# Optimization experiments

Hardware: AMD Instinct MI355X
Metric: run time of the kernel (lower is better)

Reference implementation:

```python
import jax, jax.numpy as jnp
import numpy as np

H = 16        # query heads
HK = 8        # kv heads
D = 128       # head dim
HID = 2048    # hidden size
FF = 6144     # mlp intermediate
THETA = 1e6   # rope base (qwen3)
EPS = 1e-6
T = 2048      # total tokens


def rmsnorm(x, w):
    return x * jax.lax.rsqrt(jnp.mean(x * x, axis=-1, keepdims=True) + EPS) * w


def rope(pos, x):
    # x: [T, h, D], rotate-half RoPE
    half = D // 2
    inv = 1.0 / (THETA ** (jnp.arange(half, dtype=jnp.float32) / half))
    freqs = pos.astype(jnp.float32)[:, None] * inv          # [T, half]
    cos = jnp.cos(freqs)[:, None, :]
    sin = jnp.sin(freqs)[:, None, :]
    x1, x2 = x[..., :half], x[..., half:]
    return jnp.concatenate([x1 * cos - x2 * sin, x2 * cos + x1 * sin], axis=-1)


def setup_inputs() -> dict:
    key = jax.random.key(0)
    ks = jax.random.split(key, 12)
    s = 0.02
    return {
        "positions": jnp.arange(T, dtype=jnp.int32),
        "hidden_states": jax.random.normal(ks[0], (T, HID), dtype=jnp.float32),
        "wq": jax.random.normal(ks[1], (H * D, HID), dtype=jnp.float32) * s,
        "wk": jax.random.normal(ks[2], (HK * D, HID), dtype=jnp.float32) * s,
        "wv": jax.random.normal(ks[3], (HK * D, HID), dtype=jnp.float32) * s,
        "wo": jax.random.normal(ks[4], (HID, H * D), dtype=jnp.float32) * s,
        "q_norm_w": jnp.ones((D,), dtype=jnp.float32),
        "k_norm_w": jnp.ones((D,), dtype=jnp.float32),
        "ln1_w": jnp.ones((HID,), dtype=jnp.float32),
        "ln2_w": jnp.ones((HID,), dtype=jnp.float32),
        "w_gate": jax.random.normal(ks[5], (FF, HID), dtype=jnp.float32) * s,
        "w_up": jax.random.normal(ks[6], (FF, HID), dtype=jnp.float32) * s,
        "w_down": jax.random.normal(ks[7], (HID, FF), dtype=jnp.float32) * s,
    }


def reference(positions, hidden_states, wq, wk, wv, wo, q_norm_w, k_norm_w,
              ln1_w, ln2_w, w_gate, w_up, w_down):
    t = hidden_states.shape[0]
    residual = hidden_states
    h = rmsnorm(hidden_states, ln1_w)
    q = (h @ wq.T).reshape(t, H, D)
    k = (h @ wk.T).reshape(t, HK, D)
    v = (h @ wv.T).reshape(t, HK, D)
    q = rmsnorm(q, q_norm_w)
    k = rmsnorm(k, k_norm_w)
    q = rope(positions, q)
    k = rope(positions, k)
    # GQA: expand kv heads to query heads
    g = H // HK
    kr = jnp.repeat(k, g, axis=1)  # [t, H, D]
    vr = jnp.repeat(v, g, axis=1)
    scores = jnp.einsum('thd,shd->hts', q, kr) * (D ** -0.5)
    causal = positions[:, None] >= positions[None, :]
    scores = jnp.where(causal[None], scores, jnp.finfo(scores.dtype).min)
    p = jax.nn.softmax(scores, axis=-1)
    o = jnp.einsum('hts,shd->thd', p, vr).reshape(t, H * D)
    h = residual + o @ wo.T
    residual = h
    h = rmsnorm(h, ln2_w)
    h = (jax.nn.silu(h @ w_gate.T) * (h @ w_up.T)) @ w_down.T
    return residual + h
```

## Files before the change

### kernel.cpp

```cpp
#include <hip/hip_runtime.h>
#include <hip/hip_bf16.h>
#include <stdint.h>

namespace {

constexpr int kT   = 2048;
constexpr int kHid = 2048;
constexpr int kH   = 16;
constexpr int kHK  = 8;
constexpr int kD   = 128;
constexpr int kFF  = 6144;

using bf16x8 = __attribute__((ext_vector_type(8))) short;
using f32x4  = __attribute__((ext_vector_type(4))) float;

__device__ __forceinline__ float bf2f(unsigned short u) {
    return __uint_as_float(((unsigned)u) << 16);
}
__device__ __forceinline__ unsigned short f2bf(float f) {
    unsigned u = __float_as_uint(f);
    return (unsigned short)((u + 0x7fffu + ((u >> 16) & 1u)) >> 16);
}
__device__ __forceinline__ void gload_lds16(const void* g, void* l) {
    __builtin_amdgcn_global_load_lds(
        (__attribute__((address_space(1))) void*)g,
        (__attribute__((address_space(3))) void*)l, 16, 0, 0);
}
__device__ __forceinline__ f32x4 mf(bf16x8 a, bf16x8 b, f32x4 c) {
    return __builtin_amdgcn_mfma_f32_16x16x32_bf16(a, b, c, 0, 0, 0);
}

__global__ __launch_bounds__(256)
void cvt_f32_bf16(const float* __restrict__ src, unsigned short* __restrict__ dst, int n4) {
    int i = blockIdx.x * 256 + threadIdx.x;
    if (i < n4) {
        float4 v = ((const float4*)src)[i];
        ushort4 o;
        o.x = f2bf(v.x); o.y = f2bf(v.y); o.z = f2bf(v.z); o.w = f2bf(v.w);
        ((ushort4*)dst)[i] = o;
    }
}

__global__ __launch_bounds__(256)
void reduce4(const float* __restrict__ p0, const float* __restrict__ p1,
             const float* __restrict__ p2, const float* __restrict__ p3,
             const float* __restrict__ res, float* __restrict__ out, int n4) {
    int i = blockIdx.x * 256 + threadIdx.x;
    if (i < n4) {
        float4 a = ((const float4*)p0)[i];
        float4 b = ((const float4*)p1)[i];
        float4 c = ((const float4*)p2)[i];
        float4 d = ((const float4*)p3)[i];
        float4 r = ((const float4*)res)[i];
        float4 o;
        o.x = a.x + b.x + c.x + d.x + r.x;
        o.y = a.y + b.y + c.y + d.y + r.y;
        o.z = a.z + b.z + c.z + d.z + r.z;
        o.w = a.w + b.w + c.w + d.w + r.w;
        ((float4*)out)[i] = o;
    }
}

__global__ __launch_bounds__(256)
void rmsnorm_k(const float* __restrict__ x, const float* __restrict__ w,
               unsigned short* __restrict__ out) {
    const int row = blockIdx.x;
    const int tid = threadIdx.x;
    const float4* xr = (const float4*)(x + (size_t)row * kHid);
    float4 v0 = xr[tid];
    float4 v1 = xr[tid + 256];
    float ss = v0.x*v0.x + v0.y*v0.y + v0.z*v0.z + v0.w*v0.w
             + v1.x*v1.x + v1.y*v1.y + v1.z*v1.z + v1.w*v1.w;
#pragma unroll
    for (int m = 1; m < 64; m <<= 1) ss += __shfl_xor(ss, m);
    __shared__ float red[4];
    if ((tid & 63) == 0) red[tid >> 6] = ss;
    __syncthreads();
    float tot = red[0] + red[1] + red[2] + red[3];
    float rs = rsqrtf(tot * (1.0f / kHid) + 1e-6f);
    const float4* wv = (const float4*)w;
    float4 w0 = wv[tid], w1 = wv[tid + 256];
    ushort4 o0, o1;
    o0.x = f2bf(v0.x * rs * w0.x); o0.y = f2bf(v0.y * rs * w0.y);
    o0.z = f2bf(v0.z * rs * w0.z); o0.w = f2bf(v0.w * rs * w0.w);
    o1.x = f2bf(v1.x * rs * w1.x); o1.y = f2bf(v1.y * rs * w1.y);
    o1.z = f2bf(v1.z * rs * w1.z); o1.w = f2bf(v1.w * rs * w1.w);
    ushort4* orow = (ushort4*)(out + (size_t)row * kHid);
    orow[tid] = o0;
    orow[tid + 256] = o1;
}

template <int EPI>
__global__ __launch_bounds__(512, 2)
void gemm256(const unsigned short* __restrict__ A,
             const unsigned short* __restrict__ B,
             void* __restrict__ C,
             const float* __restrict__ Res,
             const unsigned short* __restrict__ G,
             int M, int N, int K, int KS,
             float* __restrict__ p0, float* __restrict__ p1,
             float* __restrict__ p2, float* __restrict__ p3) {
    __shared__ unsigned short smem[2][4][128 * 64];

    const int tid  = threadIdx.x;
    const int lane = tid & 63;
    const int l15  = lane & 15;
    const int g4   = lane >> 4;
    const int wid  = tid >> 6;
    const int wr   = wid >> 2;
    const int wc   = wid & 3;
    const int bm   = blockIdx.y * 256;
    const int bn   = blockIdx.x * 256;
    const int kb   = (EPI == 4) ? blockIdx.z * KS : 0;
    const int NT   = ((EPI == 4) ? KS : K) >> 6;
    const int NI   = NT >> 1;

    f32x4 acc[8][4] = {};

    auto stage = [&](int b, int reg, int t) {
        const unsigned short* Base = (reg < 2) ? A : B;
        const int br = ((reg < 2) ? bm : bn) + (reg & 1) * 128;
#pragma unroll
        for (int i = 0; i < 2; ++i) {
            int ch   = tid + i * 512;
            int row  = ch >> 3;
            int slot = (ch & 7) ^ (row & 7);
            gload_lds16(Base + (size_t)(br + row) * K + kb + t * 64 + slot * 8,
                        (char*)&smem[b][reg][0] + ch * 16);
        }
    };
    auto rdA = [&](int b, int m, int ks) {
        int row = m * 16 + l15;
        return *(const bf16x8*)((const char*)&smem[b][wr][0]
               + row * 128 + (((ks * 4 + g4) ^ (row & 7)) * 16));
    };
    auto rdB = [&](int b, int n, int ks) {
        int row = wc * 64 + n * 16 + l15;
        return *(const bf16x8*)((const char*)&smem[b][2 + (row >> 7)][0]
               + (row & 127) * 128 + (((ks * 4 + g4) ^ (row & 7)) * 16));
    };

    stage(0, 2, 0); stage(0, 3, 0); stage(0, 0, 0); stage(0, 1, 0);
    stage(1, 2, 1); stage(1, 3, 1); stage(1, 0, 1);
    asm volatile("s_waitcnt vmcnt(6)" ::: "memory");
    __builtin_amdgcn_s_barrier();

    for (int i = 0; i < NI; ++i) {
        const int e  = 2 * i;
        const int o  = e + 1;
        const bool pf = (e + 2 < NT);
        bf16x8 af[4][2], bfr[4][2];

#pragma unroll
        for (int m = 0; m < 4; ++m) { af[m][0] = rdA(0, m, 0); af[m][1] = rdA(0, m, 1); }
#pragma unroll
        for (int n = 0; n < 4; ++n) { bfr[n][0] = rdB(0, n, 0); bfr[n][1] = rdB(0, n, 1); }
        stage(1, 1, o);
        __builtin_amdgcn_s_barrier();
        asm volatile("s_waitcnt lgkmcnt(0)" ::: "memory");
        __builtin_amdgcn_sched_barrier(0);
        __builtin_amdgcn_s_setprio(1);
#pragma unroll
        for (int m = 0; m < 4; ++m)
#pragma unroll
            for (int n = 0; n < 2; ++n) {
                acc[m][n] = mf(af[m][0], bfr[n][0], acc[m][n]);
                acc[m][n] = mf(af[m][1], bfr[n][1], acc[m][n]);
            }
        __builtin_amdgcn_s_setprio(0);
        __builtin_amdgcn_s_barrier();

        if (pf) stage(0, 2, e + 2);
        __builtin_amdgcn_s_barrier();
        __builtin_amdgcn_s_setprio(1);
#pragma unroll
        for (int m = 0; m < 4; ++m)
#pragma unroll
            for (int n = 2; n < 4; ++n) {
                acc[m][n] = mf(af[m][0], bfr[n][0], acc[m][n]);
                acc[m][n] = mf(af[m][1], bfr[n][1], acc[m][n]);
            }
        __builtin_amdgcn_s_setprio(0);
        __builtin_amdgcn_s_barrier();

#pragma unroll
        for (int m = 0; m < 4; ++m) { af[m][0] = rdA(0, 4 + m, 0); af[m][1] = rdA(0, 4 + m, 1); }
        if (pf) stage(0, 3, e + 2);
        __builtin_amdgcn_s_barrier();
        asm volatile("s_waitcnt lgkmcnt(0)" ::: "memory");
        __builtin_amdgcn_sched_barrier(0);
        __builtin_amdgcn_s_setprio(1);
#pragma unroll
        for (int m = 0; m < 4; ++m)
#pragma unroll
            for (int n = 0; n < 2; ++n) {
                acc[4 + m][n] = mf(af[m][0], bfr[n][0], acc[4 + m][n]);
                acc[4 + m][n] = mf(af[m][1], bfr[n][1], acc[4 + m][n]);
            }
        __builtin_amdgcn_s_setprio(0);
        __builtin_amdgcn_s_barrier();

        if (pf) stage(0, 0, e + 2);
        __builtin_amdgcn_s_barrier();
        __builtin_amdgcn_s_setprio(1);
#pragma unroll
        for (int m = 0; m < 4; ++m)
#pragma unroll
            for (int n = 2; n < 4; ++n) {
                acc[4 + m][n] = mf(af[m][0], bfr[n][0], acc[4 + m][n]);
                acc[4 + m][n] = mf(af[m][1], bfr[n][1], acc[4 + m][n]);
            }
        __builtin_amdgcn_s_setprio(0);
        if (pf) asm volatile("s_waitcnt vmcnt(6)" ::: "memory");
        else    asm volatile("s_waitcnt vmcnt(0)" ::: "memory");
        __builtin_amdgcn_s_barrier();

#pragma unroll
        for (int m = 0; m < 4; ++m) { af[m][0] = rdA(1, m, 0); af[m][1] = rdA(1, m, 1); }
#pragma unroll
        for (int n = 0; n < 4; ++n) { bfr[n][0] = rdB(1, n, 0); bfr[n][1] = rdB(1, n, 1); }
        if (pf) stage(0, 1, e + 2);
        __builtin_amdgcn_s_barrier();
        asm volatile("s_waitcnt lgkmcnt(0)" ::: "memory");
        __builtin_amdgcn_sched_barrier(0);
        __builtin_amdgcn_s_setprio(1);
#pragma unroll
        for (int m = 0; m < 4; ++m)
#pragma unroll
            for (int n = 0; n < 2; ++n) {
                acc[m][n] = mf(af[m][0], bfr[n][0], acc[m][n]);
                acc[m][n] = mf(af[m][1], bfr[n][1], acc[m][n]);
            }
        __builtin_amdgcn_s_setprio(0);
        __builtin_amdgcn_s_barrier();

        if (pf) stage(1, 2, o + 2);
        __builtin_amdgcn_s_barrier();
        __builtin_amdgcn_s_setprio(1);
#pragma unroll
        for (int m = 0; m < 4; ++m)
#pragma unroll
            for (int n = 2; n < 4; ++n) {
                acc[m][n] = mf(af[m][0], bfr[n][0], acc[m][n]);
                acc[m][n] = mf(af[m][1], bfr[n][1], acc[m][n]);
            }
        __builtin_amdgcn_s_setprio(0);
        __builtin_amdgcn_s_barrier();

#pragma unroll
        for (int m = 0; m < 4; ++m) { af[m][0] = rdA(1, 4 + m, 0); af[m][1] = rdA(1, 4 + m, 1); }
        if (pf) stage(1, 3, o + 2);
        __builtin_amdgcn_s_barrier();
        asm volatile("s_waitcnt lgkmcnt(0)" ::: "memory");
        __builtin_amdgcn_sched_barrier(0);
        __builtin_amdgcn_s_setprio(1);
#pragma unroll
        for (int m = 0; m < 4; ++m)
#pragma unroll
            for (int n = 0; n < 2; ++n) {
                acc[4 + m][n] = mf(af[m][0], bfr[n][0], acc[4 + m][n]);
                acc[4 + m][n] = mf(af[m][1], bfr[n][1], acc[4 + m][n]);
            }
        __builtin_amdgcn_s_setprio(0);
        __builtin_amdgcn_s_barrier();

        if (pf) stage(1, 0, o + 2);
        __builtin_amdgcn_s_barrier();
        __builtin_amdgcn_s_setprio(1);
#pragma unroll
        for (int m = 0; m < 4; ++m)
#pragma unroll
            for (int n = 2; n < 4; ++n) {
                acc[4 + m][n] = mf(af[m][0], bfr[n][0], acc[4 + m][n]);
                acc[4 + m][n] = mf(af[m][1], bfr[n][1], acc[4 + m][n]);
            }
        __builtin_amdgcn_s_setprio(0);
        if (pf) asm volatile("s_waitcnt vmcnt(6)" ::: "memory");
        __builtin_amdgcn_s_barrier();
    }

    float* P = nullptr;
    if (EPI == 4) {
        const int z = blockIdx.z;
        P = (z == 0) ? p0 : (z == 1) ? p1 : (z == 2) ? p2 : p3;
    }
#pragma unroll
    for (int m = 0; m < 8; ++m) {
#pragma unroll
        for (int n = 0; n < 4; ++n) {
            int row = bm + wr * 128 + m * 16 + g4 * 4;
            int col = bn + wc * 64 + n * 16 + l15;
#pragma unroll
            for (int r = 0; r < 4; ++r) {
                size_t idx = (size_t)(row + r) * N + col;
                float v = acc[m][n][r];
                if (EPI == 0) {
                    ((float*)C)[idx] = v;
                } else if (EPI == 1) {
                    ((unsigned short*)C)[idx] = f2bf(v);
                } else if (EPI == 2) {
                    ((float*)C)[idx] = v + Res[idx];
                } else if (EPI == 3) {
                    float g = bf2f(G[idx]);
                    ((unsigned short*)C)[idx] = f2bf(g / (1.0f + __expf(-g)) * v);
                } else {
                    P[idx] = v;
                }
            }
        }
    }
}

__global__ __launch_bounds__(512, 2)
void gemm_gu(const unsigned short* __restrict__ A,
             const unsigned short* __restrict__ WGp,
             const unsigned short* __restrict__ WUp,
             unsigned short* __restrict__ OUT) {
    __shared__ unsigned short smem[2][4][128 * 64];

    const int tid  = threadIdx.x;
    const int lane = tid & 63;
    const int l15  = lane & 15;
    const int g4   = lane >> 4;
    const int wid  = tid >> 6;
    const int wr   = wid >> 1;
    const int wc   = wid & 1;
    const int bm   = blockIdx.y * 256;
    const int bn2  = blockIdx.x * 128;
    const int K    = kHid;
    const int NT   = K >> 6;
    const int NI   = NT >> 1;

    f32x4 accg[4][4] = {};
    f32x4 accu[4][4] = {};

    auto stage = [&](int b, int reg, int t) {
        const unsigned short* Base = (reg == 2) ? WGp : (reg == 3) ? WUp : A;
        const int br = (reg < 2) ? (bm + reg * 128) : bn2;
#pragma unroll
        for (int i = 0; i < 2; ++i) {
            int ch   = tid + i * 512;
            int row  = ch >> 3;
            int slot = (ch & 7) ^ (row & 7);
            gload_lds16(Base + (size_t)(br + row) * K + t * 64 + slot * 8,
                        (char*)&smem[b][reg][0] + ch * 16);
        }
    };
    auto rdA = [&](int b, int m, int ks) {
        int rt  = wr * 64 + m * 16 + l15;
        int row = rt & 127;
        return *(const bf16x8*)((const char*)&smem[b][rt >> 7][0]
               + row * 128 + (((ks * 4 + g4) ^ (row & 7)) * 16));
    };
    auto rdB = [&](int b, int reg, int n, int ks) {
        int row = wc * 64 + n * 16 + l15;
        return *(const bf16x8*)((const char*)&smem[b][reg][0]
               + row * 128 + (((ks * 4 + g4) ^ (row & 7)) * 16));
    };

    stage(0, 2, 0); stage(0, 3, 0); stage(0, 0, 0); stage(0, 1, 0);
    stage(1, 2, 1); stage(1, 0, 1); stage(1, 1, 1);
    asm volatile("s_waitcnt vmcnt(6)" ::: "memory");
    __builtin_amdgcn_s_barrier();

    for (int i = 0; i < NI; ++i) {
        const int e  = 2 * i;
        const int o  = e + 1;
        const bool pf = (e + 2 < NT);
        bf16x8 af[4][2], bg[4][2], bu[4][2];

#pragma unroll
        for (int m = 0; m < 4; ++m) { af[m][0] = rdA(0, m, 0); af[m][1] = rdA(0, m, 1); }
#pragma unroll
        for (int n = 0; n < 4; ++n) { bg[n][0] = rdB(0, 2, n, 0); bg[n][1] = rdB(0, 2, n, 1); }
        stage(1, 3, o);
        __builtin_amdgcn_s_barrier();
        asm volatile("s_waitcnt lgkmcnt(0)" ::: "memory");
        __builtin_amdgcn_sched_barrier(0);
        __builtin_amdgcn_s_setprio(1);
#pragma unroll
        for (int m = 0; m < 4; ++m)
#pragma unroll
            for (int n = 0; n < 2; ++n) {
                accg[m][n] = mf(af[m][0], bg[n][0], accg[m][n]);
                accg[m][n] = mf(af[m][1], bg[n][1], accg[m][n]);
            }
        __builtin_amdgcn_s_setprio(0);
        __builtin_amdgcn_s_barrier();

        if (pf) stage(0, 2, e + 2);
        __builtin_amdgcn_s_barrier();
        __builtin_amdgcn_s_setprio(1);
#pragma unroll
        for (int m = 0; m < 4; ++m)
#pragma unroll
            for (int n = 2; n < 4; ++n) {
                accg[m][n] = mf(af[m][0], bg[n][0], accg[m][n]);
                accg[m][n] = mf(af[m][1], bg[n][1], accg[m][n]);
            }
        __builtin_amdgcn_s_setprio(0);
        __builtin_amdgcn_s_barrier();

#pragma unroll
        for (int n = 0; n < 4; ++n) { bu[n][0] = rdB(0, 3, n, 0); bu[n][1] = rdB(0, 3, n, 1); }
        if (pf) stage(0, 0, e + 2);
        __builtin_amdgcn_s_barrier();
        asm volatile("s_waitcnt lgkmcnt(0)" ::: "memory");
        __builtin_amdgcn_sched_barrier(0);
        __builtin_amdgcn_s_setprio(1);
#pragma unroll
        for (int m = 0; m < 4; ++m)
#pragma unroll
            for (int n = 0; n < 2; ++n) {
                accu[m][n] = mf(af[m][0], bu[n][0], accu[m][n]);
                accu[m][n] = mf(af[m][1], bu[n][1], accu[m][n]);
            }
        __builtin_amdgcn_s_setprio(0);
        __builtin_amdgcn_s_barrier();

        if (pf) stage(0, 1, e + 2);
        __builtin_amdgcn_s_barrier();
        __builtin_amdgcn_s_setprio(1);
#pragma unroll
        for (int m = 0; m < 4; ++m)
#pragma unroll
            for (int n = 2; n < 4; ++n) {
                accu[m][n] = mf(af[m][0], bu[n][0], accu[m][n]);
                accu[m][n] = mf(af[m][1], bu[n][1], accu[m][n]);
            }
        __builtin_amdgcn_s_setprio(0);
        if (pf) asm volatile("s_waitcnt vmcnt(6)" ::: "memory");
        else    asm volatile("s_waitcnt vmcnt(0)" ::: "memory");
        __builtin_amdgcn_s_barrier();

#pragma unroll
        for (int m = 0; m < 4; ++m) { af[m][0] = rdA(1, m, 0); af[m][1] = rdA(1, m, 1); }
#pragma unroll
        for (int n = 0; n < 4; ++n) { bg[n][0] = rdB(1, 2, n, 0); bg[n][1] = rdB(1, 2, n, 1); }
        if (pf) stage(0, 3, e + 2);
        __builtin_amdgcn_s_barrier();
        asm volatile("s_waitcnt lgkmcnt(0)" ::: "memory");
        __builtin_amdgcn_sched_barrier(0);
        __builtin_amdgcn_s_setprio(1);
#pragma unroll
        for (int m = 0; m < 4; ++m)
#pragma unroll
            for (int n = 0; n < 2; ++n) {
                accg[m][n] = mf(af[m][0], bg[n][0], accg[m][n]);
                accg[m][n] = mf(af[m][1], bg[n][1], accg[m][n]);
            }
        __builtin_amdgcn_s_setprio(0);
        __builtin_amdgcn_s_barrier();

        if (pf) stage(1, 2, o + 2);
        __builtin_amdgcn_s_barrier();
        __builtin_amdgcn_s_setprio(1);
#pragma unroll
        for (int m = 0; m < 4; ++m)
#pragma unroll
            for (int n = 2; n < 4; ++n) {
                accg[m][n] = mf(af[m][0], bg[n][0], accg[m][n]);
                accg[m][n] = mf(af[m][1], bg[n][1], accg[m][n]);
            }
        __builtin_amdgcn_s_setprio(0);
        __builtin_amdgcn_s_barrier();

#pragma unroll
        for (int n = 0; n < 4; ++n) { bu[n][0] = rdB(1, 3, n, 0); bu[n][1] = rdB(1, 3, n, 1); }
        if (pf) stage(1, 0, o + 2);
        __builtin_amdgcn_s_barrier();
        asm volatile("s_waitcnt lgkmcnt(0)" ::: "memory");
        __builtin_amdgcn_sched_barrier(0);
        __builtin_amdgcn_s_setprio(1);
#pragma unroll
        for (int m = 0; m < 4; ++m)
#pragma unroll
            for (int n = 0; n < 2; ++n) {
                accu[m][n] = mf(af[m][0], bu[n][0], accu[m][n]);
                accu[m][n] = mf(af[m][1], bu[n][1], accu[m][n]);
            }
        __builtin_amdgcn_s_setprio(0);
        __builtin_amdgcn_s_barrier();

        if (pf) stage(1, 1, o + 2);
        __builtin_amdgcn_s_barrier();
        __builtin_amdgcn_s_setprio(1);
#pragma unroll
        for (int m = 0; m < 4; ++m)
#pragma unroll
            for (int n = 2; n < 4; ++n) {
                accu[m][n] = mf(af[m][0], bu[n][0], accu[m][n]);
                accu[m][n] = mf(af[m][1], bu[n][1], accu[m][n]);
            }
        __builtin_amdgcn_s_setprio(0);
        if (pf) asm volatile("s_waitcnt vmcnt(6)" ::: "memory");
        __builtin_amdgcn_s_barrier();
    }

#pragma unroll
    for (int m = 0; m < 4; ++m) {
#pragma unroll
        for (int n = 0; n < 4; ++n) {
            int row = bm + wr * 64 + m * 16 + g4 * 4;
            int col = bn2 + wc * 64 + n * 16 + l15;
#pragma unroll
            for (int r = 0; r < 4; ++r) {
                float g = accg[m][n][r];
                float u = accu[m][n][r];
                OUT[(size_t)(row + r) * kFF + col] = f2bf(g / (1.0f + __expf(-g)) * u);
            }
        }
    }
}

__global__ __launch_bounds__(256)
void qknorm_rope(const float* __restrict__ qp0, const float* __restrict__ qp1,
                 const int* __restrict__ positions,
                 const float* __restrict__ qnw, const float* __restrict__ knw,
                 unsigned short* __restrict__ Qo, unsigned short* __restrict__ Ko) {
    const int t    = blockIdx.x;
    const int j    = blockIdx.y * 4 + (threadIdx.x >> 6);
    const int lane = threadIdx.x & 63;
    const size_t base = (size_t)t * 4096 + j * 128;
    float x1 = qp0[base + lane] + qp1[base + lane];
    float x2 = qp0[base + lane + 64] + qp1[base + lane + 64];
    float ss = x1 * x1 + x2 * x2;
#pragma unroll
    for (int m = 1; m < 64; m <<= 1) ss += __shfl_xor(ss, m);
    float rs = rsqrtf(ss * (1.0f / 128.0f) + 1e-6f);
    const float* w = (j < 16) ? qnw : knw;
    float n1 = x1 * rs * w[lane];
    float n2 = x2 * rs * w[lane + 64];
    float inv = powf(1.0e6f, -(float)lane * (1.0f / 64.0f));
    float fr = (float)positions[t] * inv;
    float sn, cs;
    sincosf(fr, &sn, &cs);
    float o1 = n1 * cs - n2 * sn;
    float o2 = n2 * cs + n1 * sn;
    if (j < 16) {
        unsigned short* d = Qo + (size_t)t * (kH * kD) + j * kD;
        d[lane] = f2bf(o1);
        d[lane + 64] = f2bf(o2);
    } else {
        unsigned short* d = Ko + (size_t)t * (kHK * kD) + (j - 16) * kD;
        d[lane] = f2bf(o1);
        d[lane + 64] = f2bf(o2);
    }
}

__global__ __launch_bounds__(256)
void vtrans(const float* __restrict__ qp0, const float* __restrict__ qp1,
            unsigned short* __restrict__ Vt) {
    __shared__ float tile[32][33];
    const int t0 = blockIdx.x * 32;
    const int d0 = blockIdx.y * 32;
    const int tc = threadIdx.x & 31;
    const int tr = threadIdx.x >> 5;
#pragma unroll
    for (int i = 0; i < 4; ++i) {
        int trow = tr + i * 8;
        size_t idx = (size_t)(t0 + trow) * 4096 + 3072 + d0 + tc;
        tile[trow][tc] = qp0[idx] + qp1[idx];
    }
    __syncthreads();
#pragma unroll
    for (int i = 0; i < 4; ++i) {
        int drow = tr + i * 8;
        Vt[(size_t)(d0 + drow) * kT + t0 + tc] = f2bf(tile[tc][drow]);
    }
}

__global__ __launch_bounds__(512, 4)
void attn_fwd5(const unsigned short* __restrict__ Q,
               const unsigned short* __restrict__ Kc,
               const unsigned short* __restrict__ Vt,
               unsigned short* __restrict__ O) {
    __shared__ unsigned short Kb[2][64 * 128];
    __shared__ unsigned short Vb[2][128 * 64];
    __shared__ float MergeML[4][2][64];

    const int tid  = threadIdx.x;
    const int lane = tid & 63;
    const int l15  = lane & 15;
    const int g4   = lane >> 4;
    const int wid  = tid >> 6;
    const int s    = wid & 1;
    const int grp  = wid >> 1;
    const int hs   = grp >> 1;
    const int qsub = grp & 1;
    const int hkk  = blockIdx.x;
    const int h    = hkk * 2 + hs;
    const int nby  = gridDim.y;
    const int by   = blockIdx.y;
    const int byl  = (by & 1) ? (nby - 1 - (by >> 1)) : (by >> 1);
    const int q0   = byl * 32 + qsub * 16;
    const int nch  = byl / 2 + 1;
    const int c0   = (nch + 1) >> 1;
    const int myn  = s ? (nch - c0) : c0;
    const int qi   = q0 + l15;
    const int vt   = grp * 64 + lane;

    const int addrA = ((g4 & 1) * 32 + l15) * 4;
    const int addrB = addrA + 64;
    const int addrQ = g4 * 80;
    const bool hb   = (g4 >> 1) != 0;

    bf16x8 qf[4];
#pragma unroll
    for (int ks = 0; ks < 4; ++ks)
        qf[ks] = *(const bf16x8*)(Q + (size_t)(q0 + l15) * (kH * kD) + h * kD + ks * 32 + g4 * 8);

    f32x4 oacc[8] = {};
    float mrun = -3e38f, lrun = 0.f;
    const float scale = 0.08838834764831845f;

    auto stage = [&](int kv0) {
#pragma unroll
        for (int i = 0; i < 4; ++i) {
            int ch  = vt + i * 256;
            int row = ch >> 4;
            int c16 = ch & 15;
            gload_lds16(Kc + (size_t)(kv0 + row) * (kHK * kD) + hkk * kD
                            + ((c16 ^ (row & 7)) * 8),
                        (char*)Kb[s] + ch * 16);
        }
#pragma unroll
        for (int i = 0; i < 4; ++i) {
            int ch  = vt + i * 256;
            int row = ch >> 3;
            int c8  = ch & 7;
            gload_lds16(Vt + (size_t)(hkk * kD + row) * kT + kv0
                            + ((c8 ^ (row & 7)) * 8),
                        (char*)Vb[s] + ch * 16);
        }
    };

    for (int c = 0; c < c0; ++c) {
        const bool act = c < myn;
        const int kv0 = (s ? (c0 + c) : c) * 64;
        if (act) stage(kv0);
        asm volatile("s_waitcnt vmcnt(0)" ::: "memory");
        __builtin_amdgcn_s_barrier();
        __builtin_amdgcn_sched_barrier(0);

        if (act) {
            f32x4 sa[4] = {};
            __builtin_amdgcn_s_setprio(1);
#pragma unroll
            for (int hh = 0; hh < 4; ++hh) {
                const int row = hh * 16 + l15;
#pragma unroll
                for (int ks = 0; ks < 4; ++ks) {
                    bf16x8 kf = *(const bf16x8*)((const char*)Kb[s]
                                  + row * 256 + (((ks * 4 + g4) ^ (row & 7)) * 16));
                    sa[hh] = mf(kf, qf[ks], sa[hh]);
                }
            }
            __builtin_amdgcn_s_setprio(0);

            float sv[4][4];
#pragma unroll
            for (int hh = 0; hh < 4; ++hh)
#pragma unroll
                for (int r = 0; r < 4; ++r)
                    sv[hh][r] = sa[hh][r] * scale;
            if (kv0 + 63 > q0) {
#pragma unroll
                for (int hh = 0; hh < 4; ++hh)
#pragma unroll
                    for (int r = 0; r < 4; ++r) {
                        int ki = kv0 + hh * 16 + g4 * 4 + r;
                        if (ki > qi) sv[hh][r] = -3e38f;
                    }
            }

            float m16;
            {
                float a = fmaxf(fmaxf(sv[0][0], sv[0][1]), fmaxf(sv[0][2], sv[0][3]));
                float b2 = fmaxf(fmaxf(sv[1][0], sv[1][1]), fmaxf(sv[1][2], sv[1][3]));
                float c2 = fmaxf(fmaxf(sv[2][0], sv[2][1]), fmaxf(sv[2][2], sv[2][3]));
                float d2 = fmaxf(fmaxf(sv[3][0], sv[3][1]), fmaxf(sv[3][2], sv[3][3]));
                m16 = fmaxf(fmaxf(a, b2), fmaxf(c2, d2));
            }
            m16 = fmaxf(m16, __shfl_xor(m16, 16));
            m16 = fmaxf(m16, __shfl_xor(m16, 32));

            if (__any(m16 > mrun)) {
                float mnew = fmaxf(mrun, m16);
                float corr = __expf(mrun - mnew);
                mrun = mnew;
                lrun *= corr;
                float cr[4];
#pragma unroll
                for (int r = 0; r < 4; ++r)
                    cr[r] = __int_as_float(__builtin_amdgcn_ds_bpermute(
                                addrQ + 4 * r, __float_as_int(corr)));
#pragma unroll
                for (int c2 = 0; c2 < 8; ++c2)
#pragma unroll
                    for (int r = 0; r < 4; ++r)
                        oacc[c2][r] *= cr[r];
            }

            float p[4][4];
            float ps = 0.f;
#pragma unroll
            for (int hh = 0; hh < 4; ++hh)
#pragma unroll
                for (int r = 0; r < 4; ++r) {
                    float pe = __expf(sv[hh][r] - mrun);
                    p[hh][r] = pe;
                    ps += pe;
                }
            ps += __shfl_xor(ps, 16);
            ps += __shfl_xor(ps, 32);
            lrun += ps;

            unsigned pk[4][2];
#pragma unroll
            for (int hh = 0; hh < 4; ++hh) {
                asm("v_cvt_pk_bf16_f32 %0, %1, %2"
                    : "=v"(pk[hh][0]) : "v"(p[hh][0]), "v"(p[hh][1]));
                asm("v_cvt_pk_bf16_f32 %0, %1, %2"
                    : "=v"(pk[hh][1]) : "v"(p[hh][2]), "v"(p[hh][3]));
            }
            int ex[4][2][2];
#pragma unroll
            for (int hh = 0; hh < 4; ++hh)
#pragma unroll
                for (int ii = 0; ii < 2; ++ii) {
                    ex[hh][ii][0] = __builtin_amdgcn_ds_bpermute(addrA, (int)pk[hh][ii]);
                    ex[hh][ii][1] = __builtin_amdgcn_ds_bpermute(addrB, (int)pk[hh][ii]);
                }
            union { int w[4]; bf16x8 v; } pu0, pu1;
#pragma unroll
            for (int jw = 0; jw < 4; ++jw) {
                pu0.w[jw] = hb ? ex[1][jw & 1][jw >> 1] : ex[0][jw & 1][jw >> 1];
                pu1.w[jw] = hb ? ex[3][jw & 1][jw >> 1] : ex[2][jw & 1][jw >> 1];
            }
            bf16x8 pa0 = pu0.v;
            bf16x8 pa1 = pu1.v;

            __builtin_amdgcn_s_setprio(1);
#pragma unroll
            for (int c2 = 0; c2 < 8; ++c2) {
                const int d = c2 * 16 + l15;
                bf16x8 vf0 = *(const bf16x8*)((const char*)Vb[s]
                              + d * 128 + ((g4 ^ (d & 7)) * 16));
                oacc[c2] = mf(pa0, vf0, oacc[c2]);
                bf16x8 vf1 = *(const bf16x8*)((const char*)Vb[s]
                              + d * 128 + ((((4 + g4) ^ (d & 7))) * 16));
                oacc[c2] = mf(pa1, vf1, oacc[c2]);
            }
            __builtin_amdgcn_s_setprio(0);
        }
        __builtin_amdgcn_s_barrier();
    }

    float* KbF = (float*)&Kb[0][0];
    if (s == 1) {
        MergeML[grp][0][lane] = mrun;
        MergeML[grp][1][lane] = lrun;
#pragma unroll
        for (int c2 = 0; c2 < 8; ++c2)
#pragma unroll
            for (int r = 0; r < 4; ++r)
                KbF[grp * 2048 + (c2 * 4 + r) * 64 + lane] = oacc[c2][r];
    }
    asm volatile("s_waitcnt lgkmcnt(0)" ::: "memory");
    __builtin_amdgcn_s_barrier();

    if (s == 0) {
        float m1 = MergeML[grp][0][lane];
        float l1 = MergeML[grp][1][lane];
        float mg = fmaxf(mrun, m1);
        float a0 = __expf(mrun - mg);
        float a1 = __expf(m1 - mg);
        float L  = lrun * a0 + l1 * a1;
        float ar0[4], ar1[4], Lr[4];
#pragma unroll
        for (int r = 0; r < 4; ++r) {
            ar0[r] = __int_as_float(__builtin_amdgcn_ds_bpermute(
                         addrQ + 4 * r, __float_as_int(a0)));
            ar1[r] = __int_as_float(__builtin_amdgcn_ds_bpermute(
                         addrQ + 4 * r, __float_as_int(a1)));
            Lr[r]  = __int_as_float(__builtin_amdgcn_ds_bpermute(
                         addrQ + 4 * r, __float_as_int(L)));
        }
#pragma unroll
        for (int c2 = 0; c2 < 8; ++c2)
#pragma unroll
            for (int r = 0; r < 4; ++r) {
                float oex = KbF[grp * 2048 + (c2 * 4 + r) * 64 + lane];
                float v = (oacc[c2][r] * ar0[r] + oex * ar1[r]) / Lr[r];
                O[(size_t)(q0 + g4 * 4 + r) * (kH * kD) + h * kD + c2 * 16 + l15] = f2bf(v);
            }
    }
}

}

extern "C" void kernel_launch(void* const* d_in, const int* in_sizes, int n_in,
                              void* d_out, int out_size, void* d_ws, size_t ws_size,
                              hipStream_t stream) {
    (void)in_sizes; (void)n_in; (void)out_size; (void)ws_size;

    const int*   positions = (const int*)  d_in[0];
    const float* hidden    = (const float*)d_in[1];
    const float* wq  = (const float*)d_in[2];
    const float* wk  = (const float*)d_in[3];
    const float* wv  = (const float*)d_in[4];
    const float* wo  = (const float*)d_in[5];
    const float* qnw = (const float*)d_in[6];
    const float* knw = (const float*)d_in[7];
    const float* ln1 = (const float*)d_in[8];
    const float* ln2 = (const float*)d_in[9];
    const float* wg  = (const float*)d_in[10];
    const float* wu  = (const float*)d_in[11];
    const float* wd  = (const float*)d_in[12];

    char* ws = (char*)d_ws;
    unsigned short* WQKV = (unsigned short*)(ws + 0);
    unsigned short* WO   = (unsigned short*)(ws + 16777216);
    unsigned short* WG   = (unsigned short*)(ws + 25165824);
    unsigned short* WU   = (unsigned short*)(ws + 50331648);
    unsigned short* WD   = (unsigned short*)(ws + 75497472);
    unsigned short* XN1  = (unsigned short*)(ws + 100663296);
    unsigned short* OATT = (unsigned short*)(ws + 109051904);
    float*          H1   = (float*)(ws + 117440512);
    unsigned short* XN2  = (unsigned short*)(ws + 134217728);
    unsigned short* QB   = (unsigned short*)(ws + 176160768);
    unsigned short* KB   = (unsigned short*)(ws + 184549376);
    unsigned short* VT   = (unsigned short*)(ws + 188743680);
    unsigned short* ACT  = (unsigned short*)(ws + 167772160);

    float* QP0 = (float*)(ws + 142606336);
    float* QP1 = (float*)(ws + 109051904);
    float* OP0 = (float*)(ws + 142606336);
    float* OP1 = (float*)(ws + 159383552);
    float* OP2 = (float*)(ws + 176160768);
    float* OP3 = (float*)(ws + 0);
    float* DP0 = (float*)(ws + 0);
    float* DP1 = (float*)(ws + 16777216);
    float* DP2 = (float*)(ws + 33554432);
    float* DP3 = (float*)(ws + 142606336);

    auto cvt = [&](const float* s, unsigned short* dst, size_t n) {
        int n4 = (int)(n / 4);
        cvt_f32_bf16<<<dim3((n4 + 255) / 256), dim3(256), 0, stream>>>(s, dst, n4);
    };

    cvt(wq, WQKV,                 (size_t)kH  * kD * kHid);
    cvt(wk, WQKV + 2048 * kHid,   (size_t)kHK * kD * kHid);
    cvt(wv, WQKV + 3072 * kHid,   (size_t)kHK * kD * kHid);
    cvt(wo, WO,                   (size_t)kHid * kH * kD);
    cvt(wg, WG,                   (size_t)kFF * kHid);
    cvt(wu, WU,                   (size_t)kFF * kHid);
    cvt(wd, WD,                   (size_t)kHid * kFF);

    rmsnorm_k<<<dim3(kT), dim3(256), 0, stream>>>(hidden, ln1, XN1);

    gemm256<4><<<dim3(4096 / 256, kT / 256, 2), dim3(512), 0, stream>>>(
        XN1, WQKV, nullptr, nullptr, nullptr, kT, 4096, kHid, 1024,
        QP0, QP1, QP0, QP0);

    qknorm_rope<<<dim3(kT, 6), dim3(256), 0, stream>>>(
        QP0, QP1, positions, qnw, knw, QB, KB);
    vtrans<<<dim3(kT / 32, 1024 / 32), dim3(256), 0, stream>>>(QP0, QP1, VT);

    attn_fwd5<<<dim3(kHK, kT / 32), dim3(512), 0, stream>>>(QB, KB, VT, OATT);

    gemm256<4><<<dim3(kHid / 256, kT / 256, 4), dim3(512), 0, stream>>>(
        OATT, WO, nullptr, nullptr, nullptr, kT, kHid, kHid, 512,
        OP0, OP1, OP2, OP3);
    reduce4<<<dim3(kT * kHid / 4 / 256), dim3(256), 0, stream>>>(
        OP0, OP1, OP2, OP3, hidden, H1, kT * kHid / 4);

    rmsnorm_k<<<dim3(kT), dim3(256), 0, stream>>>(H1, ln2, XN2);

    gemm_gu<<<dim3(kFF / 128, kT / 256), dim3(512), 0, stream>>>(XN2, WG, WU, ACT);

    gemm256<4><<<dim3(kHid / 256, kT / 256, 4), dim3(512), 0, stream>>>(
        ACT, WD, nullptr, nullptr, nullptr, kT, kHid, kFF, 1536,
        DP0, DP1, DP2, DP3);
    reduce4<<<dim3(kT * kHid / 4 / 256), dim3(256), 0, stream>>>(
        DP0, DP1, DP2, DP3, H1, (float*)d_out, kT * kHid / 4);
}
```

Baseline: 413.2 us.

## Shrink GEMM M-tile to 128 and cut split-K partials

Replaces the 256x256 split-K GEMM with a 128x256 tile variant. The QKV projection now runs without split-K and writes a single fp32 buffer directly. The O-projection and down-projection drop from four K-splits to two, so a reduce2 kernel replaces reduce4. Halving the M tile doubles the block count, which keeps parallelism while cutting partial-sum traffic and reduction work. The cost is lower data reuse per block, since each B tile is loaded for only 128 rows, and more LDS traffic relative to MFMA work.

```diff
diff --git a/kernel.cpp b/kernel.cpp
--- a/kernel.cpp
+++ b/kernel.cpp
@@ -42,21 +42,18 @@
 }
 
 __global__ __launch_bounds__(256)
-void reduce4(const float* __restrict__ p0, const float* __restrict__ p1,
-             const float* __restrict__ p2, const float* __restrict__ p3,
+void reduce2(const float* __restrict__ p0, const float* __restrict__ p1,
              const float* __restrict__ res, float* __restrict__ out, int n4) {
     int i = blockIdx.x * 256 + threadIdx.x;
     if (i < n4) {
         float4 a = ((const float4*)p0)[i];
         float4 b = ((const float4*)p1)[i];
-        float4 c = ((const float4*)p2)[i];
-        float4 d = ((const float4*)p3)[i];
         float4 r = ((const float4*)res)[i];
         float4 o;
-        o.x = a.x + b.x + c.x + d.x + r.x;
-        o.y = a.y + b.y + c.y + d.y + r.y;
-        o.z = a.z + b.z + c.z + d.z + r.z;
-        o.w = a.w + b.w + c.w + d.w + r.w;
+        o.x = a.x + b.x + r.x;
+        o.y = a.y + b.y + r.y;
+        o.z = a.z + b.z + r.z;
+        o.w = a.w + b.w + r.w;
         ((float4*)out)[i] = o;
     }
 }
@@ -92,15 +89,12 @@
 
 template <int EPI>
 __global__ __launch_bounds__(512, 2)
-void gemm256(const unsigned short* __restrict__ A,
+void gemm128(const unsigned short* __restrict__ A,
              const unsigned short* __restrict__ B,
              void* __restrict__ C,
-             const float* __restrict__ Res,
-             const unsigned short* __restrict__ G,
              int M, int N, int K, int KS,
-             float* __restrict__ p0, float* __restrict__ p1,
-             float* __restrict__ p2, float* __restrict__ p3) {
-    __shared__ unsigned short smem[2][4][128 * 64];
+             float* __restrict__ p0, float* __restrict__ p1) {
+    __shared__ unsigned short smem[2][3][128 * 64];
 
     const int tid  = threadIdx.x;
     const int lane = tid & 63;
@@ -109,17 +103,17 @@
     const int wid  = tid >> 6;
     const int wr   = wid >> 2;
     const int wc   = wid & 3;
-    const int bm   = blockIdx.y * 256;
+    const int bm   = blockIdx.y * 128;
     const int bn   = blockIdx.x * 256;
     const int kb   = (EPI == 4) ? blockIdx.z * KS : 0;
     const int NT   = ((EPI == 4) ? KS : K) >> 6;
     const int NI   = NT >> 1;
 
-    f32x4 acc[8][4] = {};
+    f32x4 acc[4][4] = {};
 
     auto stage = [&](int b, int reg, int t) {
-        const unsigned short* Base = (reg < 2) ? A : B;
-        const int br = ((reg < 2) ? bm : bn) + (reg & 1) * 128;
+        const unsigned short* Base = (reg == 0) ? A : B;
+        const int br = (reg == 0) ? bm : bn + (reg - 1) * 128;
 #pragma unroll
         for (int i = 0; i < 2; ++i) {
             int ch   = tid + i * 512;
@@ -130,19 +124,19 @@
         }
     };
     auto rdA = [&](int b, int m, int ks) {
-        int row = m * 16 + l15;
-        return *(const bf16x8*)((const char*)&smem[b][wr][0]
+        int row = wr * 64 + m * 16 + l15;
+        return *(const bf16x8*)((const char*)&smem[b][0][0]
                + row * 128 + (((ks * 4 + g4) ^ (row & 7)) * 16));
     };
     auto rdB = [&](int b, int n, int ks) {
         int row = wc * 64 + n * 16 + l15;
-        return *(const bf16x8*)((const char*)&smem[b][2 + (row >> 7)][0]
+        return *(const bf16x8*)((const char*)&smem[b][1 + (row >> 7)][0]
                + (row & 127) * 128 + (((ks * 4 + g4) ^ (row & 7)) * 16));
     };
 
-    stage(0, 2, 0); stage(0, 3, 0); stage(0, 0, 0); stage(0, 1, 0);
-    stage(1, 2, 1); stage(1, 3, 1); stage(1, 0, 1);
-    asm volatile("s_waitcnt vmcnt(6)" ::: "memory");
+    stage(0, 1, 0); stage(0, 2, 0); stage(0, 0, 0);
+    stage(1, 1, 1); stage(1, 2, 1);
+    asm volatile("s_waitcnt vmcnt(4)" ::: "memory");
     __builtin_amdgcn_s_barrier();
 
     for (int i = 0; i < NI; ++i) {
@@ -155,18 +149,27 @@
         for (int m = 0; m < 4; ++m) { af[m][0] = rdA(0, m, 0); af[m][1] = rdA(0, m, 1); }
 #pragma unroll
         for (int n = 0; n < 4; ++n) { bfr[n][0] = rdB(0, n, 0); bfr[n][1] = rdB(0, n, 1); }
-        stage(1, 1, o);
+        stage(1, 0, o);
         __builtin_amdgcn_s_barrier();
         asm volatile("s_waitcnt lgkmcnt(0)" ::: "memory");
         __builtin_amdgcn_sched_barrier(0);
         __builtin_amdgcn_s_setprio(1);
 #pragma unroll
-        for (int m = 0; m < 4; ++m)
-#pragma unroll
-            for (int n = 0; n < 2; ++n) {
-                acc[m][n] = mf(af[m][0], bfr[n][0], acc[m][n]);
-                acc[m][n] = mf(af[m][1], bfr[n][1], acc[m][n]);
-            }
+        for (int m = 0; m < 4; ++m) {
+            acc[m][0] = mf(af[m][0], bfr[0][0], acc[m][0]);
+            acc[m][0] = mf(af[m][1], bfr[0][1], acc[m][0]);
+        }
+        __builtin_amdgcn_s_setprio(0);
+        __builtin_amdgcn_s_barrier();
+
+        if (pf) stage(0, 1, e + 2);
+        __builtin_amdgcn_s_barrier();
+        __builtin_amdgcn_s_setprio(1);
+#pragma unroll
+        for (int m = 0; m < 4; ++m) {
+            acc[m][1] = mf(af[m][0], bfr[1][0], acc[m][1]);
+            acc[m][1] = mf(af[m][1], bfr[1][1], acc[m][1]);
+        }
         __builtin_amdgcn_s_setprio(0);
         __builtin_amdgcn_s_barrier();
 
@@ -174,63 +177,49 @@
         __builtin_amdgcn_s_barrier();
         __builtin_amdgcn_s_setprio(1);
 #pragma unroll
-        for (int m = 0; m < 4; ++m)
-#pragma unroll
-            for (int n = 2; n < 4; ++n) {
-                acc[m][n] = mf(af[m][0], bfr[n][0], acc[m][n]);
-                acc[m][n] = mf(af[m][1], bfr[n][1], acc[m][n]);
-            }
-        __builtin_amdgcn_s_setprio(0);
-        __builtin_amdgcn_s_barrier();
-
-#pragma unroll
-        for (int m = 0; m < 4; ++m) { af[m][0] = rdA(0, 4 + m, 0); af[m][1] = rdA(0, 4 + m, 1); }
-        if (pf) stage(0, 3, e + 2);
+        for (int m = 0; m < 4; ++m) {
+            acc[m][2] = mf(af[m][0], bfr[2][0], acc[m][2]);
+            acc[m][2] = mf(af[m][1], bfr[2][1], acc[m][2]);
+        }
+        __builtin_amdgcn_s_setprio(0);
+        __builtin_amdgcn_s_barrier();
+
+        __builtin_amdgcn_s_setprio(1);
+#pragma unroll
+        for (int m = 0; m < 4; ++m) {
+            acc[m][3] = mf(af[m][0], bfr[3][0], acc[m][3]);
+            acc[m][3] = mf(af[m][1], bfr[3][1], acc[m][3]);
+        }
+        __builtin_amdgcn_s_setprio(0);
+        if (pf) asm volatile("s_waitcnt vmcnt(4)" ::: "memory");
+        else    asm volatile("s_waitcnt vmcnt(0)" ::: "memory");
+        __builtin_amdgcn_s_barrier();
+
+#pragma unroll
+        for (int m = 0; m < 4; ++m) { af[m][0] = rdA(1, m, 0); af[m][1] = rdA(1, m, 1); }
+#pragma unroll
+        for (int n = 0; n < 4; ++n) { bfr[n][0] = rdB(1, n, 0); bfr[n][1] = rdB(1, n, 1); }
+        if (pf) stage(0, 0, e + 2);
         __builtin_amdgcn_s_barrier();
         asm volatile("s_waitcnt lgkmcnt(0)" ::: "memory");
         __builtin_amdgcn_sched_barrier(0);
         __builtin_amdgcn_s_setprio(1);
 #pragma unroll
-        for (int m = 0; m < 4; ++m)
-#pragma unroll
-            for (int n = 0; n < 2; ++n) {
-                acc[4 + m][n] = mf(af[m][0], bfr[n][0], acc[4 + m][n]);
-                acc[4 + m][n] = mf(af[m][1], bfr[n][1], acc[4 + m][n]);
-            }
-        __builtin_amdgcn_s_setprio(0);
-        __builtin_amdgcn_s_barrier();
-
-        if (pf) stage(0, 0, e + 2);
-        __builtin_amdgcn_s_barrier();
-        __builtin_amdgcn_s_setprio(1);
-#pragma unroll
-        for (int m = 0; m < 4; ++m)
-#pragma unroll
-            for (int n = 2; n < 4; ++n) {
-                acc[4 + m][n] = mf(af[m][0], bfr[n][0], acc[4 + m][n]);
-                acc[4 + m][n] = mf(af[m][1], bfr[n][1], acc[4 + m][n]);
-            }
-        __builtin_amdgcn_s_setprio(0);
-        if (pf) asm volatile("s_waitcnt vmcnt(6)" ::: "memory");
-        else    asm volatile("s_waitcnt vmcnt(0)" ::: "memory");
-        __builtin_amdgcn_s_barrier();
-
-#pragma unroll
-        for (int m = 0; m < 4; ++m) { af[m][0] = rdA(1, m, 0); af[m][1] = rdA(1, m, 1); }
-#pragma unroll
-        for (int n = 0; n < 4; ++n) { bfr[n][0] = rdB(1, n, 0); bfr[n][1] = rdB(1, n, 1); }
-        if (pf) stage(0, 1, e + 2);
-        __builtin_amdgcn_s_barrier();
-        asm volatile("s_waitcnt lgkmcnt(0)" ::: "memory");
-        __builtin_amdgcn_sched_barrier(0);
-        __builtin_amdgcn_s_setprio(1);
-#pragma unroll
-        for (int m = 0; m < 4; ++m)
-#pragma unroll
-            for (int n = 0; n < 2; ++n) {
-                acc[m][n] = mf(af[m][0], bfr[n][0], acc[m][n]);
-                acc[m][n] = mf(af[m][1], bfr[n][1], acc[m][n]);
-            }
+        for (int m = 0; m < 4; ++m) {
+            acc[m][0] = mf(af[m][0], bfr[0][0], acc[m][0]);
+            acc[m][0] = mf(af[m][1], bfr[0][1], acc[m][0]);
+        }
+        __builtin_amdgcn_s_setprio(0);
+        __builtin_amdgcn_s_barrier();
+
+        if (pf) stage(1, 1, o + 2);
+        __builtin_amdgcn_s_barrier();
+        __builtin_amdgcn_s_setprio(1);
+#pragma unroll
+        for (int m = 0; m < 4; ++m) {
+            acc[m][1] = mf(af[m][0], bfr[1][0], acc[m][1]);
+            acc[m][1] = mf(af[m][1], bfr[1][1], acc[m][1]);
+        }
         __builtin_amdgcn_s_setprio(0);
         __builtin_amdgcn_s_barrier();
 
@@ -238,74 +227,38 @@
         __builtin_amdgcn_s_barrier();
         __builtin_amdgcn_s_setprio(1);
 #pragma unroll
-        for (int m = 0; m < 4; ++m)
-#pragma unroll
-            for (int n = 2; n < 4; ++n) {
-                acc[m][n] = mf(af[m][0], bfr[n][0], acc[m][n]);
-                acc[m][n] = mf(af[m][1], bfr[n][1], acc[m][n]);
-            }
-        __builtin_amdgcn_s_setprio(0);
-        __builtin_amdgcn_s_barrier();
-
-#pragma unroll
-        for (int m = 0; m < 4; ++m) { af[m][0] = rdA(1, 4 + m, 0); af[m][1] = rdA(1, 4 + m, 1); }
-        if (pf) stage(1, 3, o + 2);
-        __builtin_amdgcn_s_barrier();
-        asm volatile("s_waitcnt lgkmcnt(0)" ::: "memory");
-        __builtin_amdgcn_sched_barrier(0);
-        __builtin_amdgcn_s_setprio(1);
-#pragma unroll
-        for (int m = 0; m < 4; ++m)
-#pragma unroll
-            for (int n = 0; n < 2; ++n) {
-                acc[4 + m][n] = mf(af[m][0], bfr[n][0], acc[4 + m][n]);
-                acc[4 + m][n] = mf(af[m][1], bfr[n][1], acc[4 + m][n]);
-            }
-        __builtin_amdgcn_s_setprio(0);
-        __builtin_amdgcn_s_barrier();
-
-        if (pf) stage(1, 0, o + 2);
-        __builtin_amdgcn_s_barrier();
-        __builtin_amdgcn_s_setprio(1);
-#pragma unroll
-        for (int m = 0; m < 4; ++m)
-#pragma unroll
-            for (int n = 2; n < 4; ++n) {
-                acc[4 + m][n] = mf(af[m][0], bfr[n][0], acc[4 + m][n]);
-                acc[4 + m][n] = mf(af[m][1], bfr[n][1], acc[4 + m][n]);
-            }
-        __builtin_amdgcn_s_setprio(0);
-        if (pf) asm volatile("s_waitcnt vmcnt(6)" ::: "memory");
+        for (int m = 0; m < 4; ++m) {
+            acc[m][2] = mf(af[m][0], bfr[2][0], acc[m][2]);
+            acc[m][2] = mf(af[m][1], bfr[2][1], acc[m][2]);
+        }
+        __builtin_amdgcn_s_setprio(0);
+        __builtin_amdgcn_s_barrier();
+
+        __builtin_amdgcn_s_setprio(1);
+#pragma unroll
+        for (int m = 0; m < 4; ++m) {
+            acc[m][3] = mf(af[m][0], bfr[3][0], acc[m][3]);
+            acc[m][3] = mf(af[m][1], bfr[3][1], acc[m][3]);
+        }
+        __builtin_amdgcn_s_setprio(0);
+        if (pf) asm volatile("s_waitcnt vmcnt(4)" ::: "memory");
         __builtin_amdgcn_s_barrier();
     }
 
     float* P = nullptr;
-    if (EPI == 4) {
-        const int z = blockIdx.z;
-        P = (z == 0) ? p0 : (z == 1) ? p1 : (z == 2) ? p2 : p3;
-    }
-#pragma unroll
-    for (int m = 0; m < 8; ++m) {
+    if (EPI == 4) P = (blockIdx.z == 0) ? p0 : p1;
+#pragma unroll
+    for (int m = 0; m < 4; ++m) {
 #pragma unroll
         for (int n = 0; n < 4; ++n) {
-            int row = bm + wr * 128 + m * 16 + g4 * 4;
+            int row = bm + wr * 64 + m * 16 + g4 * 4;
             int col = bn + wc * 64 + n * 16 + l15;
 #pragma unroll
             for (int r = 0; r < 4; ++r) {
                 size_t idx = (size_t)(row + r) * N + col;
                 float v = acc[m][n][r];
-                if (EPI == 0) {
-                    ((float*)C)[idx] = v;
-                } else if (EPI == 1) {
-                    ((unsigned short*)C)[idx] = f2bf(v);
-                } else if (EPI == 2) {
-                    ((float*)C)[idx] = v + Res[idx];
-                } else if (EPI == 3) {
-                    float g = bf2f(G[idx]);
-                    ((unsigned short*)C)[idx] = f2bf(g / (1.0f + __expf(-g)) * v);
-                } else {
-                    P[idx] = v;
-                }
+                if (EPI == 0) ((float*)C)[idx] = v;
+                else          P[idx] = v;
             }
         }
     }
@@ -514,16 +467,15 @@
 }
 
 __global__ __launch_bounds__(256)
-void qknorm_rope(const float* __restrict__ qp0, const float* __restrict__ qp1,
-                 const int* __restrict__ positions,
+void qknorm_rope(const float* __restrict__ qkv, const int* __restrict__ positions,
                  const float* __restrict__ qnw, const float* __restrict__ knw,
                  unsigned short* __restrict__ Qo, unsigned short* __restrict__ Ko) {
     const int t    = blockIdx.x;
     const int j    = blockIdx.y * 4 + (threadIdx.x >> 6);
     const int lane = threadIdx.x & 63;
-    const size_t base = (size_t)t * 4096 + j * 128;
-    float x1 = qp0[base + lane] + qp1[base + lane];
-    float x2 = qp0[base + lane + 64] + qp1[base + lane + 64];
+    const float* src = qkv + (size_t)t * 4096 + j * 128;
+    float x1 = src[lane];
+    float x2 = src[lane + 64];
     float ss = x1 * x1 + x2 * x2;
 #pragma unroll
     for (int m = 1; m < 64; m <<= 1) ss += __shfl_xor(ss, m);
@@ -549,8 +501,7 @@
 }
 
 __global__ __launch_bounds__(256)
-void vtrans(const float* __restrict__ qp0, const float* __restrict__ qp1,
-            unsigned short* __restrict__ Vt) {
+void vtrans(const float* __restrict__ qkv, unsigned short* __restrict__ Vt) {
     __shared__ float tile[32][33];
     const int t0 = blockIdx.x * 32;
     const int d0 = blockIdx.y * 32;
@@ -559,8 +510,7 @@
 #pragma unroll
     for (int i = 0; i < 4; ++i) {
         int trow = tr + i * 8;
-        size_t idx = (size_t)(t0 + trow) * 4096 + 3072 + d0 + tc;
-        tile[trow][tc] = qp0[idx] + qp1[idx];
+        tile[trow][tc] = qkv[(size_t)(t0 + trow) * 4096 + 3072 + d0 + tc];
     }
     __syncthreads();
 #pragma unroll
@@ -829,21 +779,16 @@
     unsigned short* OATT = (unsigned short*)(ws + 109051904);
     float*          H1   = (float*)(ws + 117440512);
     unsigned short* XN2  = (unsigned short*)(ws + 134217728);
+    float*          QKVF = (float*)(ws + 142606336);
     unsigned short* QB   = (unsigned short*)(ws + 176160768);
     unsigned short* KB   = (unsigned short*)(ws + 184549376);
     unsigned short* VT   = (unsigned short*)(ws + 188743680);
     unsigned short* ACT  = (unsigned short*)(ws + 167772160);
 
-    float* QP0 = (float*)(ws + 142606336);
-    float* QP1 = (float*)(ws + 109051904);
     float* OP0 = (float*)(ws + 142606336);
     float* OP1 = (float*)(ws + 159383552);
-    float* OP2 = (float*)(ws + 176160768);
-    float* OP3 = (float*)(ws + 0);
     float* DP0 = (float*)(ws + 0);
     float* DP1 = (float*)(ws + 16777216);
-    float* DP2 = (float*)(ws + 33554432);
-    float* DP3 = (float*)(ws + 142606336);
 
     auto cvt = [&](const float* s, unsigned short* dst, size_t n) {
         int n4 = (int)(n / 4);
@@ -860,29 +805,25 @@
 
     rmsnorm_k<<<dim3(kT), dim3(256), 0, stream>>>(hidden, ln1, XN1);
 
-    gemm256<4><<<dim3(4096 / 256, kT / 256, 2), dim3(512), 0, stream>>>(
-        XN1, WQKV, nullptr, nullptr, nullptr, kT, 4096, kHid, 1024,
-        QP0, QP1, QP0, QP0);
-
-    qknorm_rope<<<dim3(kT, 6), dim3(256), 0, stream>>>(
-        QP0, QP1, positions, qnw, knw, QB, KB);
-    vtrans<<<dim3(kT / 32, 1024 / 32), dim3(256), 0, stream>>>(QP0, QP1, VT);
+    gemm128<0><<<dim3(4096 / 256, kT / 128), dim3(512), 0, stream>>>(
+        XN1, WQKV, QKVF, kT, 4096, kHid, kHid, nullptr, nullptr);
+
+    qknorm_rope<<<dim3(kT, 6), dim3(256), 0, stream>>>(QKVF, positions, qnw, knw, QB, KB);
+    vtrans<<<dim3(kT / 32, 1024 / 32), dim3(256), 0, stream>>>(QKVF, VT);
 
     attn_fwd5<<<dim3(kHK, kT / 32), dim3(512), 0, stream>>>(QB, KB, VT, OATT);
 
-    gemm256<4><<<dim3(kHid / 256, kT / 256, 4), dim3(512), 0, stream>>>(
-        OATT, WO, nullptr, nullptr, nullptr, kT, kHid, kHid, 512,
-        OP0, OP1, OP2, OP3);
-    reduce4<<<dim3(kT * kHid / 4 / 256), dim3(256), 0, stream>>>(
-        OP0, OP1, OP2, OP3, hidden, H1, kT * kHid / 4);
+    gemm128<4><<<dim3(kHid / 256, kT / 128, 2), dim3(512), 0, stream>>>(
+        OATT, WO, nullptr, kT, kHid, kHid, 1024, OP0, OP1);
+    reduce2<<<dim3(kT * kHid / 4 / 256), dim3(256), 0, stream>>>(
+        OP0, OP1, hidden, H1, kT * kHid / 4);
 
     rmsnorm_k<<<dim3(kT), dim3(256), 0, stream>>>(H1, ln2, XN2);
 
     gemm_gu<<<dim3(kFF / 128, kT / 256), dim3(512), 0, stream>>>(XN2, WG, WU, ACT);
 
-    gemm256<4><<<dim3(kHid / 256, kT / 256, 4), dim3(512), 0, stream>>>(
-        ACT, WD, nullptr, nullptr, nullptr, kT, kHid, kFF, 1536,
-        DP0, DP1, DP2, DP3);
-    reduce4<<<dim3(kT * kHid / 4 / 256), dim3(256), 0, stream>>>(
-        DP0, DP1, DP2, DP3, H1, (float*)d_out, kT * kHid / 4);
-}
+    gemm128<4><<<dim3(kHid / 256, kT / 128, 2), dim3(512), 0, stream>>>(
+        ACT, WD, nullptr, kT, kHid, kFF, 3072, DP0, DP1);
+    reduce2<<<dim3(kT * kHid / 4 / 256), dim3(256), 0, stream>>>(
+        DP0, DP1, H1, (float*)d_out, kT * kHid / 4);
+}
```

Result: faster. 396.6 us (-4.0%).
